# Kernel optimization log

Measured on AMD Instinct MI355X. Metric: run time of the kernel, lower is better.

## Reference

```python
import jax, jax.numpy as jnp
import numpy as np

B, T, SEQ = 8, 129, 128
H, N, NL, NE, V = 512, 64, 4, 128, 18

def _gelu(x):
    return jax.nn.gelu(x, approximate=False)

def _conv2d(x, w, b, stride):
    y = jax.lax.conv_general_dilated(x, w, (stride, stride), 'VALID',
                                     dimension_numbers=('NCHW', 'OIHW', 'NCHW'))
    return y + b[None, :, None, None]

def _layernorm(x, g, b, eps=1e-5):
    mu = jnp.mean(x, axis=-1, keepdims=True)
    var = jnp.mean(jnp.square(x - mu), axis=-1, keepdims=True)
    return (x - mu) * jax.lax.rsqrt(var + eps) * g + b

def _s4_kernel(log_dt, A_re, A_im, C_re, C_im, L):
    # Diagonal SSM (ZOH discretization, B=1): K[h,l] = 2*Re(sum_n Ceff * exp(dt*A)^l)
    dt = jnp.exp(log_dt)[:, None]                  # [H,1]
    A = A_re + 1j * A_im                            # [H,N] complex64
    dtA = (dt * A).astype(jnp.complex64)
    C = (C_re + 1j * C_im).astype(jnp.complex64)
    Ceff = C * (jnp.exp(dtA) - 1.0) / A             # [H,N]
    vand = jnp.exp(dtA[:, :, None] * jnp.arange(L, dtype=jnp.float32))  # [H,N,L]
    return 2.0 * jnp.einsum('hn,hnl->hl', Ceff, vand).real

def _fft_conv(u, K, D):
    # u: [B,H,L]  K: [H,L]  causal conv via zero-padded FFT
    L = u.shape[-1]
    n = 2 * L
    Uf = jnp.fft.rfft(u, n=n)
    Kf = jnp.fft.rfft(K, n=n)
    y = jnp.fft.irfft(Uf * Kf[None], n=n)[..., :L]
    return y + D[None, :, None] * u

def setup_inputs() -> dict:
    key = jax.random.key(0)
    ks = jax.random.split(key, 32)
    d = {}
    d['states'] = jax.random.uniform(ks[0], (B, T, 4, 84, 84), dtype=jnp.float32)
    d['actions'] = jax.random.randint(ks[1], (B, T), 0, V)
    d['rtgs'] = jax.random.uniform(ks[2], (B, T, 1), dtype=jnp.float32)
    s = 0.02
    d['enc_w1'] = jax.random.normal(ks[3], (32, 4, 8, 8)) * s
    d['enc_b1'] = jnp.zeros((32,))
    d['enc_w2'] = jax.random.normal(ks[4], (64, 32, 4, 4)) * s
    d['enc_b2'] = jnp.zeros((64,))
    d['enc_w3'] = jax.random.normal(ks[5], (64, 64, 3, 3)) * s
    d['enc_b3'] = jnp.zeros((64,))
    d['enc_lw'] = jax.random.normal(ks[6], (3136, NE)) * s
    d['enc_lb'] = jnp.zeros((NE,))
    d['ret_w'] = jax.random.normal(ks[7], (1, NE)) * s
    d['ret_b'] = jnp.zeros((NE,))
    d['act_emb'] = jax.random.normal(ks[8], (V, NE)) * s
    d['proj_w'] = jax.random.normal(ks[9], (3 * NE, H)) * s
    d['proj_b'] = jnp.zeros((H,))
    d['pre_w'] = jax.random.normal(ks[10], (H, H)) * s
    d['pre_b'] = jnp.zeros((H,))
    d['ln_g'] = jnp.ones((NL, H))
    d['ln_b'] = jnp.zeros((NL, H))
    lo, hi = np.log(1e-3), np.log(1e-1)
    d['log_dt'] = lo + jax.random.uniform(ks[11], (NL, H)) * (hi - lo)
    d['A_re'] = -0.5 * jnp.ones((NL, H, N))
    d['A_im'] = jnp.broadcast_to(np.pi * jnp.arange(N, dtype=jnp.float32), (NL, H, N)).copy()
    d['C_re'] = jax.random.normal(ks[12], (NL, H, N)) * (0.5 ** 0.5)
    d['C_im'] = jax.random.normal(ks[13], (NL, H, N)) * (0.5 ** 0.5)
    d['Dp'] = jax.random.normal(ks[14], (NL, H))
    d['aft_w'] = jax.random.normal(ks[15], (NL, H, H)) * s
    d['aft_b'] = jnp.zeros((NL, H))
    d['out_w'] = jax.random.normal(ks[16], (H, V)) * s
    return d

def reference(states, actions, rtgs, enc_w1, enc_b1, enc_w2, enc_b2, enc_w3, enc_b3,
              enc_lw, enc_lb, ret_w, ret_b, act_emb, proj_w, proj_b, pre_w, pre_b,
              ln_g, ln_b, log_dt, A_re, A_im, C_re, C_im, Dp, aft_w, aft_b, out_w):
    S = actions.shape[1] - 1  # del_r = 1
    # state encoder over B*S frames
    x = states[:, 1:].reshape(-1, 4, 84, 84)
    x = jax.nn.relu(_conv2d(x, enc_w1, enc_b1, 4))
    x = jax.nn.relu(_conv2d(x, enc_w2, enc_b2, 2))
    x = jax.nn.relu(_conv2d(x, enc_w3, enc_b3, 1))
    se = jnp.tanh(x.reshape(x.shape[0], -1) @ enc_lw + enc_lb)          # [B*S, NE]
    ae = jnp.tanh(act_emb[actions[:, :S].reshape(-1)])                   # [B*S, NE]
    re = jnp.tanh(rtgs[:, :S].reshape(-1, 1) @ ret_w + ret_b)            # [B*S, NE]
    u = jnp.concatenate([se, ae, re], axis=-1) @ proj_w + proj_b
    u = u.reshape(states.shape[0], S, H)
    y = _gelu(u) @ pre_w + pre_b                                          # beforeblock
    for i in range(NL):
        r = _layernorm(y, ln_g[i], ln_b[i])
        v = jnp.transpose(r, (0, 2, 1))                                   # [B,H,S]
        K = _s4_kernel(log_dt[i], A_re[i], A_im[i], C_re[i], C_im[i], S)
        c = _fft_conv(v, K, Dp[i])
        c = jnp.transpose(c, (0, 2, 1))                                   # [B,S,H]
        c = _gelu(_gelu(c) @ aft_w[i] + aft_b[i])
        y = c + y                                                          # s4_resnet
    logits = y @ out_w                                                     # [B,S,V]
    return logits
```

## Files before the change

### kernel.cpp

```cpp
#include <hip/hip_runtime.h>

#define Bq 8
#define Tq 129
#define Sq 128
#define Hq 512
#define Nq 64
#define NLq 4
#define NEq 128
#define Vq 18

typedef unsigned short u16;
typedef unsigned int u32;
typedef __attribute__((ext_vector_type(8))) short short8v;
typedef __attribute__((ext_vector_type(4))) float f32x4;

__device__ __forceinline__ float gelu_f(float x) {
  return 0.5f * x * (1.0f + erff(x * 0.70710678118654752f));
}

__device__ __forceinline__ u16 f2b(float x) {
  union { float f; unsigned int u; } v; v.f = x;
  unsigned int r = v.u + 0x7FFFu + ((v.u >> 16) & 1u);
  return (u16)(r >> 16);
}

__device__ __forceinline__ float b2f_lo(u32 u) {
  union { unsigned int u; float f; } v; v.u = u << 16; return v.f;
}
__device__ __forceinline__ float b2f_hi(u32 u) {
  union { unsigned int u; float f; } v; v.u = u & 0xffff0000u; return v.f;
}

__global__ __launch_bounds__(256) void prep_k(
    const float* __restrict__ enc_lw, const float* __restrict__ proj_w,
    const float* __restrict__ pre_w, const float* __restrict__ aft_w,
    const float* __restrict__ out_w,
    const float* __restrict__ w1, const float* __restrict__ w2,
    const float* __restrict__ w3,
    u16* __restrict__ Wt_enc, u16* __restrict__ Wt_proj, u16* __restrict__ Wt_pre,
    u16* __restrict__ Wt_aft, u16* __restrict__ Wt_out,
    u16* __restrict__ B1t, u16* __restrict__ B2t, u16* __restrict__ B3t) {
  __shared__ u16 T[64][65];
  int bid = blockIdx.x;
  if (bid >= 474) {
    int i = (bid - 474) * 256 + threadIdx.x;
    if (i < 8192) {
      int n = i >> 8, k = i & 255;
      int ic = k >> 6, ky = (k >> 3) & 7, kx = k & 7;
      B1t[i] = f2b(w1[((n * 4 + ic) * 8 + ky) * 8 + kx]);
    } else if (i < 8192 + 32768) {
      int j = i - 8192;
      int n = j >> 9, k = j & 511;
      int kyx = k >> 5, ic = k & 31, ky = kyx >> 2, kx = kyx & 3;
      B2t[j] = f2b(w2[((n * 32 + ic) * 4 + ky) * 4 + kx]);
    } else if (i < 8192 + 32768 + 36864) {
      int j = i - 40960;
      int n = j / 576, k = j - n * 576;
      int ic = k & 63, kyx = k >> 6, ky = kyx / 3, kx = kyx % 3;
      B3t[j] = f2b(w3[((n * 64 + ic) * 3 + ky) * 3 + kx]);
    }
    return;
  }
  const float* src; u16* dst; int K, N, kt, nt, t;
  if (bid < 98)       { t = bid;       src = enc_lw; dst = Wt_enc;  K = 3136; N = 128; kt = t >> 1; nt = t & 1; }
  else if (bid < 146) { t = bid - 98;  src = proj_w; dst = Wt_proj; K = 384;  N = 512; kt = t >> 3; nt = t & 7; }
  else if (bid < 210) { t = bid - 146; src = pre_w;  dst = Wt_pre;  K = 512;  N = 512; kt = t >> 3; nt = t & 7; }
  else if (bid < 466) { t = bid - 210; int L = t >> 6; t &= 63;
                        src = aft_w + (size_t)L * 262144; dst = Wt_aft + (size_t)L * 262144;
                        K = 512; N = 512; kt = t >> 3; nt = t & 7; }
  else                { t = bid - 466; src = out_w;  dst = Wt_out;  K = 512;  N = 18;  kt = t;      nt = 0; }
  int k0 = kt * 64, n0 = nt * 64;
  #pragma unroll
  for (int it = 0; it < 16; it++) {
    int idx = it * 256 + threadIdx.x;
    int rr = idx >> 6, cc = idx & 63;
    float v = (n0 + cc < N) ? src[(size_t)(k0 + rr) * N + n0 + cc] : 0.f;
    T[cc][rr] = f2b(v);
  }
  __syncthreads();
  #pragma unroll
  for (int it = 0; it < 16; it++) {
    int idx = it * 256 + threadIdx.x;
    int rr = idx >> 6, cc = idx & 63;
    dst[(size_t)(n0 + rr) * K + k0 + cc] = T[rr][cc];
  }
}

__global__ __launch_bounds__(512) void conv1_mfma(const float* __restrict__ states,
    const u16* __restrict__ B1t, const float* __restrict__ bias, u16* __restrict__ out) {
  __shared__ u16 lds[28224];
  int fr = blockIdx.x;
  int b = fr >> 7, s = fr & 127;
  const float* in = states + (size_t)(b * Tq + s + 1) * 28224;
  int tid = threadIdx.x;
  float4 stg[14];
  #pragma unroll
  for (int it = 0; it < 14; it++) {
    int idx = tid + it * 512;
    if (idx < 7056) stg[it] = ((const float4*)in)[idx];
  }
  #pragma unroll
  for (int it = 0; it < 14; it++) {
    int idx = tid + it * 512;
    if (idx < 7056) {
      ushort4 uv;
      uv.x = f2b(stg[it].x); uv.y = f2b(stg[it].y);
      uv.z = f2b(stg[it].z); uv.w = f2b(stg[it].w);
      *(ushort4*)&lds[idx * 4] = uv;
    }
  }
  int lane = tid & 63, w = tid >> 6;
  int q = lane >> 4, r = lane & 15;
  short8v bfr[2][8];
  #pragma unroll
  for (int nt = 0; nt < 2; nt++)
    #pragma unroll
    for (int ks = 0; ks < 8; ks++)
      bfr[nt][ks] = *(const short8v*)(B1t + (nt * 16 + r) * 256 + ks * 32 + q * 8);
  __syncthreads();
  for (int mt = w; mt < 25; mt += 8) {
    int m = mt * 16 + r;
    int oy = m / 20, ox = m % 20;
    f32x4 acc0 = {0.f, 0.f, 0.f, 0.f}, acc1 = {0.f, 0.f, 0.f, 0.f};
    #pragma unroll
    for (int ks = 0; ks < 8; ks++) {
      int k0 = ks * 32 + q * 8;
      int ic = k0 >> 6, ky = (k0 >> 3) & 7;
      int ai = ic * 7056 + (oy * 4 + ky) * 84 + ox * 4;
      ushort4 lo = *(const ushort4*)&lds[ai];
      ushort4 hi = *(const ushort4*)&lds[ai + 4];
      short8v av;
      av[0] = (short)lo.x; av[1] = (short)lo.y; av[2] = (short)lo.z; av[3] = (short)lo.w;
      av[4] = (short)hi.x; av[5] = (short)hi.y; av[6] = (short)hi.z; av[7] = (short)hi.w;
      acc0 = __builtin_amdgcn_mfma_f32_16x16x32_bf16(av, bfr[0][ks], acc0, 0, 0, 0);
      acc1 = __builtin_amdgcn_mfma_f32_16x16x32_bf16(av, bfr[1][ks], acc1, 0, 0, 0);
    }
    #pragma unroll
    for (int reg = 0; reg < 4; reg++) {
      int pos = mt * 16 + q * 4 + reg;
      out[(size_t)fr * 12800 + pos * 32 + r]      = f2b(fmaxf(acc0[reg] + bias[r], 0.f));
      out[(size_t)fr * 12800 + pos * 32 + 16 + r] = f2b(fmaxf(acc1[reg] + bias[16 + r], 0.f));
    }
  }
}

__global__ __launch_bounds__(256) void conv23_mfma(const u16* __restrict__ o1,
    const u16* __restrict__ B2t, const u16* __restrict__ B3t,
    const float* __restrict__ b2, const float* __restrict__ b3,
    u16* __restrict__ x3b) {
  __shared__ u16 o1l[12800];
  __shared__ u16 o2l[5184];
  int fr = blockIdx.x;
  int tid = threadIdx.x;
  const short8v* src = (const short8v*)(o1 + (size_t)fr * 12800);
  short8v* dst = (short8v*)o1l;
  #pragma unroll
  for (int it = 0; it < 7; it++) {
    int idx = tid + it * 256;
    if (idx < 1600) dst[idx] = src[idx];
  }
  int lane = tid & 63, w = tid >> 6;
  int q = lane >> 4, r = lane & 15;
  int n = w * 16 + r;
  short8v bfr2[16];
  #pragma unroll
  for (int ks = 0; ks < 16; ks++)
    bfr2[ks] = *(const short8v*)(B2t + n * 512 + ks * 32 + q * 8);
  __syncthreads();
  float bn2 = b2[n];
  #pragma unroll
  for (int mt = 0; mt < 6; mt++) {
    int m = mt * 16 + r; if (m > 80) m = 80;
    int oy = m / 9, ox = m % 9;
    f32x4 acc = {0.f, 0.f, 0.f, 0.f};
    #pragma unroll
    for (int ks = 0; ks < 16; ks++) {
      int ky = ks >> 2, kx = ks & 3;
      int ai = ((oy * 2 + ky) * 20 + ox * 2 + kx) * 32 + q * 8;
      short8v av = *(const short8v*)&o1l[ai];
      acc = __builtin_amdgcn_mfma_f32_16x16x32_bf16(av, bfr2[ks], acc, 0, 0, 0);
    }
    #pragma unroll
    for (int reg = 0; reg < 4; reg++) {
      int pos = mt * 16 + q * 4 + reg;
      if (pos < 81)
        o2l[pos * 64 + n] = f2b(fmaxf(acc[reg] + bn2, 0.f));
    }
  }
  short8v bfr3[18];
  #pragma unroll
  for (int ks = 0; ks < 18; ks++)
    bfr3[ks] = *(const short8v*)(B3t + n * 576 + ks * 32 + q * 8);
  __syncthreads();
  float bn3 = b3[n];
  #pragma unroll
  for (int mt = 0; mt < 4; mt++) {
    int m = mt * 16 + r; if (m > 48) m = 48;
    int oy = m / 7, ox = m % 7;
    f32x4 acc = {0.f, 0.f, 0.f, 0.f};
    #pragma unroll
    for (int ks = 0; ks < 18; ks++) {
      int kyx = ks >> 1;
      int ky = kyx / 3, kx = kyx % 3;
      int ic0 = (ks & 1) * 32 + q * 8;
      int ai = ((oy + ky) * 9 + ox + kx) * 64 + ic0;
      short8v av = *(const short8v*)&o2l[ai];
      acc = __builtin_amdgcn_mfma_f32_16x16x32_bf16(av, bfr3[ks], acc, 0, 0, 0);
    }
    #pragma unroll
    for (int reg = 0; reg < 4; reg++) {
      int pos = mt * 16 + q * 4 + reg;
      if (pos < 49)
        x3b[(size_t)fr * 3136 + n * 49 + pos] = f2b(fmaxf(acc[reg] + bn3, 0.f));
    }
  }
}

template<bool AF32, int EPI, bool STATS>
__global__ __launch_bounds__(256) void mgemm(const void* __restrict__ Av,
    const u16* __restrict__ Wt, const float* __restrict__ bias,
    const float* __restrict__ res, void* __restrict__ Cv,
    float2* __restrict__ part, int M, int K, int N, int ldc) {
  __shared__ u16 As[4][64][40];
  __shared__ u16 Bs[4][64][40];
  int tid = threadIdx.x;
  int bn = blockIdx.x * 64, bm = blockIdx.y * 64;
  int lane = tid & 63, w = tid >> 6;
  int q = lane >> 4, r = lane & 15;
  int wm = (w >> 1) * 32, wn = (w & 1) * 32;
  int am = tid >> 2, ak0 = (tid & 3) * 8;
  f32x4 acc[2][2] = {};
  for (int k0 = 0; k0 < K; k0 += 128) {
    #pragma unroll
    for (int st = 0; st < 4; st++) {
      int kk = k0 + st * 32 + ak0;
      if constexpr (AF32) {
        const float* A = (const float*)Av;
        const float* src = A + (size_t)(bm + am) * K + kk;
        float4 v0 = *(const float4*)src;
        float4 v1 = *(const float4*)(src + 4);
        ushort4 lo, hi;
        lo.x = f2b(v0.x); lo.y = f2b(v0.y); lo.z = f2b(v0.z); lo.w = f2b(v0.w);
        hi.x = f2b(v1.x); hi.y = f2b(v1.y); hi.z = f2b(v1.z); hi.w = f2b(v1.w);
        *(ushort4*)&As[st][am][ak0] = lo;
        *(ushort4*)&As[st][am][ak0 + 4] = hi;
      } else {
        *(short8v*)&As[st][am][ak0] =
            *(const short8v*)((const u16*)Av + (size_t)(bm + am) * K + kk);
      }
      *(short8v*)&Bs[st][am][ak0] = *(const short8v*)(Wt + (size_t)(bn + am) * K + kk);
    }
    __syncthreads();
    #pragma unroll
    for (int st = 0; st < 4; st++) {
      short8v a0 = *(const short8v*)&As[st][wm + r][q * 8];
      short8v a1 = *(const short8v*)&As[st][wm + 16 + r][q * 8];
      short8v b0 = *(const short8v*)&Bs[st][wn + r][q * 8];
      short8v b1 = *(const short8v*)&Bs[st][wn + 16 + r][q * 8];
      acc[0][0] = __builtin_amdgcn_mfma_f32_16x16x32_bf16(a0, b0, acc[0][0], 0, 0, 0);
      acc[0][1] = __builtin_amdgcn_mfma_f32_16x16x32_bf16(a0, b1, acc[0][1], 0, 0, 0);
      acc[1][0] = __builtin_amdgcn_mfma_f32_16x16x32_bf16(a1, b0, acc[1][0], 0, 0, 0);
      acc[1][1] = __builtin_amdgcn_mfma_f32_16x16x32_bf16(a1, b1, acc[1][1], 0, 0, 0);
    }
    __syncthreads();
  }
  float yv[2][2][4];
  #pragma unroll
  for (int ms = 0; ms < 2; ms++) {
    #pragma unroll
    for (int ns = 0; ns < 2; ns++) {
      #pragma unroll
      for (int reg = 0; reg < 4; reg++) {
        int m = bm + wm + ms * 16 + q * 4 + reg;
        int n = bn + wn + ns * 16 + r;
        if (n < N) {
          float v = acc[ms][ns][reg] + (bias ? bias[n] : 0.f);
          if (EPI == 0) { ((float*)Cv)[(size_t)m * ldc + n] = v; yv[ms][ns][reg] = v; }
          if (EPI == 2) ((u16*)Cv)[(size_t)m * ldc + n] = f2b(gelu_f(v));
          if (EPI == 3) {
            float o = gelu_f(v) + res[(size_t)m * ldc + n];
            ((float*)Cv)[(size_t)m * ldc + n] = o; yv[ms][ns][reg] = o;
          }
        }
      }
    }
  }
  if constexpr (STATS) {
    #pragma unroll
    for (int ms = 0; ms < 2; ms++) {
      #pragma unroll
      for (int reg = 0; reg < 4; reg++) {
        float s = yv[ms][0][reg] + yv[ms][1][reg];
        float s2 = yv[ms][0][reg] * yv[ms][0][reg] + yv[ms][1][reg] * yv[ms][1][reg];
        #pragma unroll
        for (int o = 1; o <= 8; o <<= 1) {
          s += __shfl_xor(s, o);
          s2 += __shfl_xor(s2, o);
        }
        if (r == 0) {
          int m = bm + wm + ms * 16 + q * 4 + reg;
          part[(size_t)(blockIdx.x * 2 + (w & 1)) * 1024 + m] = make_float2(s, s2);
        }
      }
    }
  }
}

__global__ __launch_bounds__(256) void enc_gemm(const u16* __restrict__ A,
    const u16* __restrict__ Wt, float* __restrict__ Cp) {
  __shared__ u16 As[64][40];
  __shared__ u16 Bs[64][40];
  int tid = threadIdx.x;
  int bn = blockIdx.x * 64, bm = blockIdx.y * 64, kc = blockIdx.z;
  int lane = tid & 63, w = tid >> 6;
  int q = lane >> 4, r = lane & 15;
  int wm = (w >> 1) * 32, wn = (w & 1) * 32;
  int am = tid >> 2, ak = (tid & 3) * 8;
  f32x4 acc[2][2] = {};
  int kend = kc * 448 + 448;
  for (int k0 = kc * 448; k0 < kend; k0 += 32) {
    *(short8v*)&As[am][ak] = *(const short8v*)(A + (size_t)(bm + am) * 3136 + k0 + ak);
    *(short8v*)&Bs[am][ak] = *(const short8v*)(Wt + (size_t)(bn + am) * 3136 + k0 + ak);
    __syncthreads();
    short8v a0 = *(const short8v*)&As[wm + r][q * 8];
    short8v a1 = *(const short8v*)&As[wm + 16 + r][q * 8];
    short8v b0 = *(const short8v*)&Bs[wn + r][q * 8];
    short8v b1 = *(const short8v*)&Bs[wn + 16 + r][q * 8];
    acc[0][0] = __builtin_amdgcn_mfma_f32_16x16x32_bf16(a0, b0, acc[0][0], 0, 0, 0);
    acc[0][1] = __builtin_amdgcn_mfma_f32_16x16x32_bf16(a0, b1, acc[0][1], 0, 0, 0);
    acc[1][0] = __builtin_amdgcn_mfma_f32_16x16x32_bf16(a1, b0, acc[1][0], 0, 0, 0);
    acc[1][1] = __builtin_amdgcn_mfma_f32_16x16x32_bf16(a1, b1, acc[1][1], 0, 0, 0);
    __syncthreads();
  }
  #pragma unroll
  for (int ms = 0; ms < 2; ms++)
    #pragma unroll
    for (int ns = 0; ns < 2; ns++)
      #pragma unroll
      for (int reg = 0; reg < 4; reg++) {
        int m = bm + wm + ms * 16 + q * 4 + reg;
        int n = bn + wn + ns * 16 + r;
        Cp[(size_t)(kc * 1024 + m) * 128 + n] = acc[ms][ns][reg];
      }
}

__global__ __launch_bounds__(256) void embedred_k(const float* __restrict__ Cp,
    const float* __restrict__ enc_lb, const int* __restrict__ actions,
    const float* __restrict__ rtgs, const float* __restrict__ act_emb,
    const float* __restrict__ ret_w, const float* __restrict__ ret_b,
    u16* __restrict__ uin) {
  int f = blockIdx.x;
  int b = f >> 7, s = f & 127;
  int e = threadIdx.x;
  if (e < 128) {
    float sum = enc_lb[e];
    #pragma unroll
    for (int kc = 0; kc < 7; kc++) sum += Cp[(size_t)(kc * 1024 + f) * 128 + e];
    uin[(size_t)f * 384 + e] = f2b(tanhf(sum));
    uin[(size_t)f * 384 + 256 + e] =
        f2b(tanhf(fmaf(rtgs[b * Tq + s], ret_w[e], ret_b[e])));
  } else {
    int ee = e - 128;
    int a = actions[b * Tq + s];
    uin[(size_t)f * 384 + 128 + ee] = f2b(tanhf(act_emb[a * NEq + ee]));
  }
}

__global__ __launch_bounds__(64) void s4k_gen(const float* __restrict__ log_dt,
    const float* __restrict__ A_re, const float* __restrict__ A_im,
    const float* __restrict__ C_re, const float* __restrict__ C_im,
    u16* __restrict__ Ktb) {
  __shared__ float con[64][129];
  int lh = blockIdx.x;
  int n = threadIdx.x;
  float dt = expf(log_dt[lh]);
  float ar = A_re[(size_t)lh * Nq + n], ai = A_im[(size_t)lh * Nq + n];
  float al = dt * ar, be = dt * ai;
  float er = expf(al);
  float wr = er * cosf(be), wi = er * sinf(be);
  float zr = wr - 1.0f, zi = wi;
  float den = 1.0f / (ar * ar + ai * ai);
  float tr = (zr * ar + zi * ai) * den, ti = (zi * ar - zr * ai) * den;
  float Cr = C_re[(size_t)lh * Nq + n], Ci = C_im[(size_t)lh * Nq + n];
  float cr = Cr * tr - Ci * ti, ci = Cr * ti + Ci * tr;
  float curr = 1.0f, curi = 0.0f;
  for (int l = 0; l < Sq; l++) {
    con[n][l] = cr * curr - ci * curi;
    float nr = curr * wr - curi * wi;
    curi = curr * wi + curi * wr;
    curr = nr;
  }
  __syncthreads();
  int layer = lh >> 9, h = lh & 511;
  #pragma unroll
  for (int li = n; li < Sq; li += 64) {
    float s = 0.f;
    for (int j = 0; j < 64; j++) s += con[j][li];
    Ktb[((size_t)layer * Sq + li) * Hq + h] = f2b(2.0f * s);
  }
}

__global__ __launch_bounds__(256) void sconv_fused(const float* __restrict__ y,
    const float2* __restrict__ part, const float* __restrict__ g,
    const float* __restrict__ bta, const u16* __restrict__ Kt,
    const float* __restrict__ D, u16* __restrict__ cact) {
  __shared__ u32 P[16][140];
  __shared__ u32 KL[16][132];
  __shared__ float2 statl[128];
  int hc = blockIdx.x, b = blockIdx.y;
  int t = threadIdx.x;
  int h0 = hc * 32;
  if (t < 128) {
    float s = 0.f, s2 = 0.f;
    #pragma unroll
    for (int pc = 0; pc < 16; pc++) {
      float2 pp = part[(size_t)pc * 1024 + b * Sq + t];
      s += pp.x; s2 += pp.y;
    }
    float mu = s * (1.f / Hq);
    float var = s2 * (1.f / Hq) - mu * mu;
    statl[t] = make_float2(mu, rsqrtf(var + 1e-5f));
  }
  if (t < 16) {
    #pragma unroll
    for (int i = 0; i < 8; i++) P[t][i] = 0;
  }
  #pragma unroll
  for (int it = 0; it < 8; it++) {
    int idx = it * 256 + t;
    int p = idx & 15, j = idx >> 4;
    KL[p][j] = *(const u32*)(Kt + (size_t)j * Hq + h0 + 2 * p);
  }
  __syncthreads();
  #pragma unroll
  for (int it = 0; it < 8; it++) {
    int idx = it * 256 + t;
    int p = idx & 15, s = idx >> 4;
    int row = b * Sq + s;
    float2 v = *(const float2*)(y + (size_t)row * Hq + h0 + 2 * p);
    float2 st = statl[s];
    float2 gg = *(const float2*)(g + h0 + 2 * p);
    float2 bb = *(const float2*)(bta + h0 + 2 * p);
    float r0 = (v.x - st.x) * st.y * gg.x + bb.x;
    float r1 = (v.y - st.x) * st.y * gg.y + bb.y;
    P[p][8 + s] = (u32)f2b(r0) | ((u32)f2b(r1) << 16);
  }
  __syncthreads();
  int p = t & 15, sg = t >> 4;
  int s0 = sg * 8;
  float acc0[8], acc1[8];
  float2 d2 = *(const float2*)(D + h0 + 2 * p);
  #pragma unroll
  for (int k = 0; k < 8; k++) {
    u32 rv = P[p][8 + s0 + k];
    acc0[k] = d2.x * b2f_lo(rv);
    acc1[k] = d2.y * b2f_hi(rv);
  }
  for (int jb = 0; jb <= sg; jb++) {
    int base = (sg - jb) * 8;
    u32 wv[16], kv[8];
    *(uint4*)&wv[0]  = *(const uint4*)&P[p][base];
    *(uint4*)&wv[4]  = *(const uint4*)&P[p][base + 4];
    *(uint4*)&wv[8]  = *(const uint4*)&P[p][base + 8];
    *(uint4*)&wv[12] = *(const uint4*)&P[p][base + 12];
    *(uint4*)&kv[0]  = *(const uint4*)&KL[p][jb * 8];
    *(uint4*)&kv[4]  = *(const uint4*)&KL[p][jb * 8 + 4];
    float wlo[16], whi[16], klo[8], khi[8];
    #pragma unroll
    for (int i = 0; i < 16; i++) { wlo[i] = b2f_lo(wv[i]); whi[i] = b2f_hi(wv[i]); }
    #pragma unroll
    for (int i = 0; i < 8; i++) { klo[i] = b2f_lo(kv[i]); khi[i] = b2f_hi(kv[i]); }
    #pragma unroll
    for (int jo = 0; jo < 8; jo++)
      #pragma unroll
      for (int k = 0; k < 8; k++) {
        acc0[k] = fmaf(klo[jo], wlo[8 + k - jo], acc0[k]);
        acc1[k] = fmaf(khi[jo], whi[8 + k - jo], acc1[k]);
      }
  }
  #pragma unroll
  for (int k = 0; k < 8; k++) {
    int s = s0 + k;
    u32 outv = (u32)f2b(gelu_f(acc0[k])) | ((u32)f2b(gelu_f(acc1[k])) << 16);
    *(u32*)(cact + ((size_t)(b * Sq + s)) * Hq + h0 + 2 * p) = outv;
  }
}

extern "C" void kernel_launch(void* const* d_in, const int* in_sizes, int n_in,
                              void* d_out, int out_size, void* d_ws, size_t ws_size,
                              hipStream_t stream) {
  const float* states  = (const float*)d_in[0];
  const int*   actions = (const int*)  d_in[1];
  const float* rtgs    = (const float*)d_in[2];
  const float* enc_w1  = (const float*)d_in[3];
  const float* enc_b1  = (const float*)d_in[4];
  const float* enc_w2  = (const float*)d_in[5];
  const float* enc_b2  = (const float*)d_in[6];
  const float* enc_w3  = (const float*)d_in[7];
  const float* enc_b3  = (const float*)d_in[8];
  const float* enc_lw  = (const float*)d_in[9];
  const float* enc_lb  = (const float*)d_in[10];
  const float* ret_w   = (const float*)d_in[11];
  const float* ret_b   = (const float*)d_in[12];
  const float* act_emb = (const float*)d_in[13];
  const float* proj_w  = (const float*)d_in[14];
  const float* proj_b  = (const float*)d_in[15];
  const float* pre_w   = (const float*)d_in[16];
  const float* pre_b   = (const float*)d_in[17];
  const float* ln_g    = (const float*)d_in[18];
  const float* ln_b    = (const float*)d_in[19];
  const float* log_dt  = (const float*)d_in[20];
  const float* A_re    = (const float*)d_in[21];
  const float* A_im    = (const float*)d_in[22];
  const float* C_re    = (const float*)d_in[23];
  const float* C_im    = (const float*)d_in[24];
  const float* Dp      = (const float*)d_in[25];
  const float* aft_w   = (const float*)d_in[26];
  const float* aft_b   = (const float*)d_in[27];
  const float* out_w   = (const float*)d_in[28];

  u16* Wt_enc  = (u16*)d_ws;
  u16* Wt_proj = Wt_enc + 401408;
  u16* Wt_pre  = Wt_proj + 196608;
  u16* Wt_aft  = Wt_pre + 262144;
  u16* Wt_out  = Wt_aft + 1048576;
  u16* B1t = Wt_out + 32768;
  u16* B2t = B1t + 8192;
  u16* B3t = B2t + 32768;
  u16* o1  = B3t + 36864;
  u16* x3b = o1 + 13107200;
  u16* uin = x3b + 3211264;
  u16* uact = uin + 393216;
  u16* cact = uact + 524288;
  u16* Ktb  = cact + 524288;
  float* y    = (float*)(Ktb + 262144);
  float* Cp   = y + 524288;
  float2* part = (float2*)(Cp + 917504);

  prep_k<<<778, 256, 0, stream>>>(enc_lw, proj_w, pre_w, aft_w, out_w,
                                  enc_w1, enc_w2, enc_w3,
                                  Wt_enc, Wt_proj, Wt_pre, Wt_aft, Wt_out,
                                  B1t, B2t, B3t);
  conv1_mfma<<<1024, 512, 0, stream>>>(states, B1t, enc_b1, o1);
  conv23_mfma<<<1024, 256, 0, stream>>>(o1, B2t, B3t, enc_b2, enc_b3, x3b);
  enc_gemm<<<dim3(2, 16, 7), 256, 0, stream>>>(x3b, Wt_enc, Cp);
  embedred_k<<<1024, 256, 0, stream>>>(Cp, enc_lb, actions, rtgs, act_emb,
                                       ret_w, ret_b, uin);
  mgemm<false, 2, false><<<dim3(8, 16), 256, 0, stream>>>(uin, Wt_proj, proj_b,
      nullptr, uact, nullptr, 1024, 384, 512, 512);
  mgemm<false, 0, true><<<dim3(8, 16), 256, 0, stream>>>(uact, Wt_pre, pre_b,
      nullptr, y, part, 1024, 512, 512, 512);
  s4k_gen<<<2048, 64, 0, stream>>>(log_dt, A_re, A_im, C_re, C_im, Ktb);

  for (int i = 0; i < NLq; i++) {
    sconv_fused<<<dim3(16, 8), 256, 0, stream>>>(y, part, ln_g + i * Hq,
                                                 ln_b + i * Hq,
                                                 Ktb + (size_t)i * Sq * Hq,
                                                 Dp + i * Hq, cact);
    mgemm<false, 3, true><<<dim3(8, 16), 256, 0, stream>>>(cact,
        Wt_aft + (size_t)i * Hq * Hq, aft_b + i * Hq, y, y, part,
        1024, 512, 512, 512);
  }
  mgemm<true, 0, false><<<dim3(1, 16), 256, 0, stream>>>(y, Wt_out, nullptr,
      nullptr, (float*)d_out, nullptr, 1024, 512, Vq, Vq);
}
```

Baseline: 217.2 us.

## Split conv1 per frame into four row-quarter blocks with packed interleaved stores

Each frame's conv1 now runs as four 256-thread blocks, each staging only the input rows needed for 5 output rows. This cuts LDS per block and raises occupancy and parallelism. Outputs are written as packed 32-bit pairs with channels interleaved, and the conv2 weight transpose is permuted to match. The cost is redundant halo loads of input rows and weight fragments reloaded inside the loop instead of held in registers.

```diff
diff --git a/kernel.cpp b/kernel.cpp
--- a/kernel.cpp
+++ b/kernel.cpp
@@ -51,7 +51,8 @@
     } else if (i < 8192 + 32768) {
       int j = i - 8192;
       int n = j >> 9, k = j & 511;
-      int kyx = k >> 5, ic = k & 31, ky = kyx >> 2, kx = kyx & 3;
+      int kyx = k >> 5, icS = k & 31, ky = kyx >> 2, kx = kyx & 3;
+      int ic = (icS & 1) ? (16 + (icS >> 1)) : (icS >> 1);
       B2t[j] = f2b(w2[((n * 32 + ic) * 4 + ky) * 4 + kx]);
     } else if (i < 8192 + 32768 + 36864) {
       int j = i - 40960;
@@ -86,60 +87,66 @@
   }
 }
 
-__global__ __launch_bounds__(512) void conv1_mfma(const float* __restrict__ states,
+__global__ __launch_bounds__(256) void conv1_mfma(const float* __restrict__ states,
     const u16* __restrict__ B1t, const float* __restrict__ bias, u16* __restrict__ out) {
-  __shared__ u16 lds[28224];
-  int fr = blockIdx.x;
+  __shared__ u16 lds[4][2016];
+  int blk = blockIdx.x;
+  int fr = blk >> 2, qt = blk & 3;
   int b = fr >> 7, s = fr & 127;
   const float* in = states + (size_t)(b * Tq + s + 1) * 28224;
   int tid = threadIdx.x;
-  float4 stg[14];
-  #pragma unroll
-  for (int it = 0; it < 14; it++) {
-    int idx = tid + it * 512;
-    if (idx < 7056) stg[it] = ((const float4*)in)[idx];
-  }
-  #pragma unroll
-  for (int it = 0; it < 14; it++) {
-    int idx = tid + it * 512;
-    if (idx < 7056) {
+  float4 stg[8];
+  #pragma unroll
+  for (int it = 0; it < 8; it++) {
+    int idx = tid + it * 256;
+    if (idx < 2016) {
+      int c = idx / 504, r2 = idx - c * 504;
+      stg[it] = ((const float4*)(in + c * 7056))[420 * qt + r2];
+    }
+  }
+  #pragma unroll
+  for (int it = 0; it < 8; it++) {
+    int idx = tid + it * 256;
+    if (idx < 2016) {
+      int c = idx / 504, r2 = idx - c * 504;
       ushort4 uv;
       uv.x = f2b(stg[it].x); uv.y = f2b(stg[it].y);
       uv.z = f2b(stg[it].z); uv.w = f2b(stg[it].w);
-      *(ushort4*)&lds[idx * 4] = uv;
+      *(ushort4*)&lds[c][r2 * 4] = uv;
     }
   }
   int lane = tid & 63, w = tid >> 6;
   int q = lane >> 4, r = lane & 15;
-  short8v bfr[2][8];
-  #pragma unroll
-  for (int nt = 0; nt < 2; nt++)
-    #pragma unroll
-    for (int ks = 0; ks < 8; ks++)
-      bfr[nt][ks] = *(const short8v*)(B1t + (nt * 16 + r) * 256 + ks * 32 + q * 8);
-  __syncthreads();
-  for (int mt = w; mt < 25; mt += 8) {
-    int m = mt * 16 + r;
-    int oy = m / 20, ox = m % 20;
+  float bn0 = bias[r], bn1 = bias[16 + r];
+  __syncthreads();
+  for (int mt = w; mt < 7; mt += 4) {
+    int m = mt * 16 + r; if (m > 99) m = 99;
+    int oyl = m / 20, ox = m % 20;
     f32x4 acc0 = {0.f, 0.f, 0.f, 0.f}, acc1 = {0.f, 0.f, 0.f, 0.f};
     #pragma unroll
     for (int ks = 0; ks < 8; ks++) {
       int k0 = ks * 32 + q * 8;
-      int ic = k0 >> 6, ky = (k0 >> 3) & 7;
-      int ai = ic * 7056 + (oy * 4 + ky) * 84 + ox * 4;
-      ushort4 lo = *(const ushort4*)&lds[ai];
-      ushort4 hi = *(const ushort4*)&lds[ai + 4];
+      int c = k0 >> 6, ky = (k0 >> 3) & 7;
+      int ai = (oyl * 4 + ky) * 84 + ox * 4;
+      ushort4 lo = *(const ushort4*)&lds[c][ai];
+      ushort4 hi = *(const ushort4*)&lds[c][ai + 4];
       short8v av;
       av[0] = (short)lo.x; av[1] = (short)lo.y; av[2] = (short)lo.z; av[3] = (short)lo.w;
       av[4] = (short)hi.x; av[5] = (short)hi.y; av[6] = (short)hi.z; av[7] = (short)hi.w;
-      acc0 = __builtin_amdgcn_mfma_f32_16x16x32_bf16(av, bfr[0][ks], acc0, 0, 0, 0);
-      acc1 = __builtin_amdgcn_mfma_f32_16x16x32_bf16(av, bfr[1][ks], acc1, 0, 0, 0);
+      short8v bv0 = *(const short8v*)(B1t + r * 256 + ks * 32 + q * 8);
+      short8v bv1 = *(const short8v*)(B1t + (16 + r) * 256 + ks * 32 + q * 8);
+      acc0 = __builtin_amdgcn_mfma_f32_16x16x32_bf16(av, bv0, acc0, 0, 0, 0);
+      acc1 = __builtin_amdgcn_mfma_f32_16x16x32_bf16(av, bv1, acc1, 0, 0, 0);
     }
     #pragma unroll
     for (int reg = 0; reg < 4; reg++) {
       int pos = mt * 16 + q * 4 + reg;
-      out[(size_t)fr * 12800 + pos * 32 + r]      = f2b(fmaxf(acc0[reg] + bias[r], 0.f));
-      out[(size_t)fr * 12800 + pos * 32 + 16 + r] = f2b(fmaxf(acc1[reg] + bias[16 + r], 0.f));
+      if (pos < 100) {
+        int gp = qt * 100 + pos;
+        u32 pk = (u32)f2b(fmaxf(acc0[reg] + bn0, 0.f)) |
+                 ((u32)f2b(fmaxf(acc1[reg] + bn1, 0.f)) << 16);
+        *(u32*)&out[(size_t)fr * 12800 + gp * 32 + 2 * r] = pk;
+      }
     }
   }
 }
@@ -541,7 +548,7 @@
                                   enc_w1, enc_w2, enc_w3,
                                   Wt_enc, Wt_proj, Wt_pre, Wt_aft, Wt_out,
                                   B1t, B2t, B3t);
-  conv1_mfma<<<1024, 512, 0, stream>>>(states, B1t, enc_b1, o1);
+  conv1_mfma<<<4096, 256, 0, stream>>>(states, B1t, enc_b1, o1);
   conv23_mfma<<<1024, 256, 0, stream>>>(o1, B2t, B3t, enc_b2, enc_b3, x3b);
   enc_gemm<<<dim3(2, 16, 7), 256, 0, stream>>>(x3b, Wt_enc, Cp);
   embedred_k<<<1024, 256, 0, stream>>>(Cp, enc_lb, actions, rtgs, act_emb,
```

Result: slower. 229.1 us (+5.5%).
